# Kernel tuning notes

Hardware: AMD Instinct MI355X
Metric: run time of the kernel (lower is better)

The kernel has to match this reference:

```python
import jax, jax.numpy as jnp
import numpy as np

N = 131072   # number of points
C = 128      # channels
H = 8        # heads
D = C // H   # head dim = 16
K = 48       # patch (window) size
P = 3000     # number of path segments


def _build_indices():
    """Faithful numpy replica of PathAttention.get_padding_and_inverse (index-only, no_grad)."""
    rng = np.random.default_rng(0)
    lengths = rng.integers(K + 1, 3 * K, size=P)          # all > K -> padded to multiple of K
    M = int(lengths.sum())
    bpad = ((lengths + K - 1) // K) * K
    off = np.concatenate([[0], np.cumsum(lengths)])
    offp = np.concatenate([[0], np.cumsum(bpad)])
    Mpad = int(offp[-1])
    pad = np.arange(Mpad)
    unpad = np.arange(M)
    for i in range(P):
        o0, o1, p0, p1 = off[i], off[i + 1], offp[i], offp[i + 1]
        unpad[o0:o1] += p0 - o0
        b = int(lengths[i])
        if b != bpad[i]:
            r = b % K
            # replicate previous window's tail into the padded region
            pad[p1 - K + r:p1] = pad[p1 - 2 * K + r:p1 - K]
        pad[p0:p1] -= p0 - o0
    # every point appears at least once so the scatter-mean covers all N rows
    inv = np.concatenate([rng.permutation(N), rng.integers(0, N, M - N)])
    rng.shuffle(inv)
    return pad, unpad, inv


def setup_inputs() -> dict:
    pad, unpad, inv = _build_indices()
    M = unpad.shape[0]
    key = jax.random.key(0)
    ks = jax.random.split(key, 8)
    s = 0.02
    theta = jax.random.uniform(ks[1], (M, D), minval=0.0, maxval=2.0 * np.pi)
    return {
        "feat": jax.random.normal(ks[0], (N, C), jnp.float32),
        "cos": jnp.cos(theta).astype(jnp.float32),
        "sin": jnp.sin(theta).astype(jnp.float32),
        "g1": jnp.ones((C,), jnp.float32),
        "b1": jnp.zeros((C,), jnp.float32),
        "qkv_w": (jax.random.normal(ks[2], (3 * C, C)) * s).astype(jnp.float32),
        "qkv_b": jnp.zeros((3 * C,), jnp.float32),
        "proj_w": (jax.random.normal(ks[3], (C, C)) * s).astype(jnp.float32),
        "proj_b": jnp.zeros((C,), jnp.float32),
        "g2": jnp.ones((C,), jnp.float32),
        "b2": jnp.zeros((C,), jnp.float32),
        "fc1_w": (jax.random.normal(ks[4], (4 * C, C)) * s).astype(jnp.float32),
        "fc1_b": jnp.zeros((4 * C,), jnp.float32),
        "fc2_w": (jax.random.normal(ks[5], (C, 4 * C)) * s).astype(jnp.float32),
        "fc2_b": jnp.zeros((C,), jnp.float32),
        "path_inverse": jnp.asarray(inv, jnp.int32),
        "pad": jnp.asarray(pad, jnp.int32),
        "unpad": jnp.asarray(unpad, jnp.int32),
        "num_heads": H,
        "patch_size": K,
    }


def _ln(x, g, b):
    m = x.mean(-1, keepdims=True)
    v = x.var(-1, keepdims=True)
    return (x - m) / jnp.sqrt(v + 1e-5) * g + b


def reference(feat, cos, sin, g1, b1, qkv_w, qkv_b, proj_w, proj_b, g2, b2,
              fc1_w, fc1_b, fc2_w, fc2_b, path_inverse, pad, unpad,
              num_heads, patch_size):
    Np, Cc = feat.shape
    Hh = num_heads
    Dd = Cc // Hh
    Kk = patch_size
    # pre-norm + qkv projection, then path gather and pad gather
    h = _ln(feat, g1, b1)
    qkv = (h @ qkv_w.T + qkv_b)[path_inverse][pad]          # [Mpad, 3C]
    Mpad = qkv.shape[0]
    qkv = qkv.reshape(Mpad, 3, Hh, Dd)
    q, k, v = qkv[:, 0], qkv[:, 1], qkv[:, 2]               # [Mpad, H, D]
    # non-interleaved rope (flash-attn apply_rotary_emb with cos of dim D//2)
    cp = cos[pad][:, :Dd // 2][:, None, :]                  # [Mpad, 1, D/2]
    sp = sin[pad][:, :Dd // 2][:, None, :]
    def rope(x):
        x1, x2 = x[..., :Dd // 2], x[..., Dd // 2:]
        return jnp.concatenate([x1 * cp - x2 * sp, x2 * cp + x1 * sp], axis=-1)
    q = rope(q)
    k = rope(k)
    # windowed attention: all windows are exactly K after padding
    Wn = Mpad // Kk
    qw = q.reshape(Wn, Kk, Hh, Dd)
    kw = k.reshape(Wn, Kk, Hh, Dd)
    vw = v.reshape(Wn, Kk, Hh, Dd)
    scores = jnp.einsum('wqhd,wkhd->whqk', qw, kw) * (Dd ** -0.5)
    p = jax.nn.softmax(scores, axis=-1)
    o = jnp.einsum('whqk,wkhd->wqhd', p, vw).reshape(Mpad, Cc)
    # unpad gather, output projection, scatter-mean combine over overlapping paths
    o = o[unpad] @ proj_w.T + proj_b                        # [M, C]
    sums = jax.ops.segment_sum(o, path_inverse, num_segments=Np)
    cnt = jax.ops.segment_sum(jnp.ones((o.shape[0],), o.dtype), path_inverse, num_segments=Np)
    a = sums / jnp.maximum(cnt, 1.0)[:, None]
    x = feat + a
    # MLP branch
    h2 = _ln(x, g2, b2)
    m = jax.nn.gelu(h2 @ fc1_w.T + fc1_b, approximate=False) @ fc2_w.T + fc2_b
    return x + m
```

## Files before the change

### kernel.cpp

```cpp
#include <hip/hip_runtime.h>


typedef __attribute__((ext_vector_type(4))) float f32x4;
typedef __attribute__((ext_vector_type(8))) short bf16x8;
typedef __attribute__((ext_vector_type(4))) short bf16x4;
typedef __attribute__((ext_vector_type(2))) unsigned u32x2;

#define MFMA(a, b, c) __builtin_amdgcn_mfma_f32_16x16x32_bf16(a, b, c, 0, 0, 0)

static __device__ __forceinline__ short f2bf(float x) {
  union { float f; unsigned u; } v; v.f = x;
  unsigned r = v.u + 0x7FFFu + ((v.u >> 16) & 1u);
  return (short)(r >> 16);
}
static __device__ __forceinline__ float bf2f(short b) {
  union { unsigned u; float f; } v;
  v.u = ((unsigned)(unsigned short)b) << 16;
  return v.f;
}
static __device__ __forceinline__ unsigned cvt_pk_bf16(float lo, float hi) {
  unsigned r;
  asm("v_cvt_pk_bf16_f32 %0, %1, %2" : "=v"(r) : "v"(lo), "v"(hi));
  return r;
}
static __device__ __forceinline__ float exp2_f(float x) {
  float r; asm("v_exp_f32 %0, %1" : "=v"(r) : "v"(x)); return r;
}
static __device__ __forceinline__ float max3_f(float a, float b, float c) {
  float r; asm("v_max3_f32 %0, %1, %2, %3" : "=v"(r) : "v"(a), "v"(b), "v"(c));
  return r;
}

static __device__ __forceinline__ float gelu_f(float v) {
  float e = exp2_f(v * -2.4554669f);
  return v * __builtin_amdgcn_rcpf(1.0f + e);
}

__global__ void k_cvt(const float* __restrict__ s, short* __restrict__ d, int n) {
  int i = blockIdx.x * 256 + threadIdx.x;
  if (i < n) d[i] = f2bf(s[i]);
}

__global__ void k_pack_w1(const float* __restrict__ w, short* __restrict__ d) {
  int i = blockIdx.x * 256 + threadIdx.x;
  int j = i & 7;  int r = i >> 3;
  int g = r & 3;  r >>= 2;
  int u = r & 15; r >>= 4;
  int kk = r & 3; int t = r >> 2;
  d[i] = f2bf(w[(t * 16 + u) * 128 + kk * 32 + g * 8 + j]);
}

__global__ void k_pack_b1(const float* __restrict__ b, float* __restrict__ d) {
  int i = blockIdx.x * 256 + threadIdx.x;
  if (i < 512) {
    int reg = i & 3; int r = i >> 2;
    int g = r & 3;   int t = r >> 2;
    d[i] = b[16 * t + 4 * g + reg];
  }
}

__global__ void k_cnt(const int* __restrict__ pinv, int* __restrict__ cnt, int M) {
  int i = blockIdx.x * 256 + threadIdx.x;
  if (i < M) atomicAdd(&cnt[pinv[i]], 1);
}

__global__ __launch_bounds__(256) void k_scan1(const int* __restrict__ cnt,
                                               int* __restrict__ lpre,
                                               int* __restrict__ bsum) {
  const int i = blockIdx.x * 256 + threadIdx.x;
  const int t = threadIdx.x, lane = t & 63, wid = t >> 6;
  int v = cnt[i];
  int x = v;
#pragma unroll
  for (int d = 1; d < 64; d <<= 1) {
    int y = __shfl_up(x, d);
    if (lane >= d) x += y;
  }
  __shared__ int wsum[4];
  if (lane == 63) wsum[wid] = x;
  __syncthreads();
  int add = 0;
#pragma unroll
  for (int wv = 0; wv < 4; wv++) add += (wv < wid) ? wsum[wv] : 0;
  lpre[i] = x + add - v;
  if (t == 255) bsum[blockIdx.x] = x + add;
}

__global__ __launch_bounds__(512) void k_scan2(int* __restrict__ bsum, int nb) {
  const int t = threadIdx.x, lane = t & 63, wid = t >> 6;
  int v = (t < nb) ? bsum[t] : 0;
  int x = v;
#pragma unroll
  for (int d = 1; d < 64; d <<= 1) {
    int y = __shfl_up(x, d);
    if (lane >= d) x += y;
  }
  __shared__ int wsum[8];
  if (lane == 63) wsum[wid] = x;
  __syncthreads();
  int add = 0;
#pragma unroll
  for (int wv = 0; wv < 8; wv++) add += (wv < wid) ? wsum[wv] : 0;
  if (t < nb) bsum[t] = x + add - v;
}

__global__ void k_place(const int* __restrict__ pinv, const int* __restrict__ lpre,
                        const int* __restrict__ bsum, int* __restrict__ cursor,
                        int* __restrict__ idxl, int M) {
  int m = blockIdx.x * 256 + threadIdx.x;
  if (m < M) {
    int n = pinv[m];
    int slot = atomicAdd(&cursor[n], 1);
    idxl[lpre[n] + bsum[n >> 8] + slot] = m;
  }
}

__global__ __launch_bounds__(256) void k1_ln_qkv(
    const float* __restrict__ feat, const float* __restrict__ g1,
    const float* __restrict__ b1, const short* __restrict__ wq,
    const float* __restrict__ bq, short* __restrict__ qkvb) {
  __shared__ short h_lds[32 * 128];
  __shared__ short o_st[32 * 384];
  const int blk = blockIdx.x, t = threadIdx.x;
  {
    const int r = t >> 3, oct = t & 7;
    const float* fp = feat + (size_t)(blk * 32 + r) * 128 + oct * 16;
    float vals[16];
    float s = 0.f, s2 = 0.f;
#pragma unroll
    for (int i = 0; i < 4; i++) {
      f32x4 v = *(const f32x4*)(fp + i * 4);
#pragma unroll
      for (int j = 0; j < 4; j++) { float x = v[j]; vals[i * 4 + j] = x; s += x; s2 += x * x; }
    }
    s += __shfl_xor(s, 1);  s += __shfl_xor(s, 2);  s += __shfl_xor(s, 4);
    s2 += __shfl_xor(s2, 1); s2 += __shfl_xor(s2, 2); s2 += __shfl_xor(s2, 4);
    float mean = s * (1.f / 128.f);
    float rstd = rsqrtf(s2 * (1.f / 128.f) - mean * mean + 1e-5f);
    const int sw = (r & 7) << 4;
#pragma unroll
    for (int gi = 0; gi < 2; gi++) {
      bf16x8 wv;
#pragma unroll
      for (int j = 0; j < 8; j++) {
        int c = oct * 16 + gi * 8 + j;
        wv[j] = f2bf((vals[gi * 8 + j] - mean) * rstd * g1[c] + b1[c]);
      }
      *(bf16x8*)((char*)h_lds + r * 256 + ((oct * 32 + gi * 16) ^ sw)) = wv;
    }
  }
  __syncthreads();
  const int wave = t >> 6, lane = t & 63, u = lane & 15, g = lane >> 4;
  f32x4 acc[2][6];
  f32x4 zz = {0.f, 0.f, 0.f, 0.f};
#pragma unroll
  for (int a = 0; a < 2; a++)
#pragma unroll
    for (int b = 0; b < 6; b++) acc[a][b] = zz;
#pragma unroll
  for (int kk = 0; kk < 4; kk++) {
    bf16x8 af[2];
#pragma unroll
    for (int rt = 0; rt < 2; rt++)
      af[rt] = *(const bf16x8*)((char*)h_lds + (rt * 16 + u) * 256 +
                                ((kk * 64 + g * 16) ^ ((u & 7) << 4)));
    bf16x8 bfr[6];
#pragma unroll
    for (int ct = 0; ct < 6; ct++) {
      int col = wave * 96 + ct * 16 + u;
      bfr[ct] = *(const bf16x8*)(wq + (size_t)col * 128 + kk * 32 + g * 8);
    }
#pragma unroll
    for (int rt = 0; rt < 2; rt++)
#pragma unroll
      for (int ct = 0; ct < 6; ct++) acc[rt][ct] = MFMA(af[rt], bfr[ct], acc[rt][ct]);
  }
#pragma unroll
  for (int rt = 0; rt < 2; rt++)
#pragma unroll
    for (int ct = 0; ct < 6; ct++) {
      int col = wave * 96 + ct * 16 + u;
      float bias = bq[col];
#pragma unroll
      for (int reg = 0; reg < 4; reg++) {
        int rowl = rt * 16 + 4 * g + reg;
        *(short*)((char*)o_st + rowl * 768 + ((col * 2) ^ (g << 5))) =
            f2bf(acc[rt][ct][reg] + bias);
      }
    }
  __syncthreads();
  for (int idx = t; idx < 1536; idx += 256) {
    int r = idx / 48, c8 = idx % 48;
    bf16x8 v = *(const bf16x8*)((char*)o_st + r * 768 +
                                ((c8 * 16) ^ ((((r >> 2) & 3)) << 5)));
    *(bf16x8*)(qkvb + ((size_t)blk * 32 + r) * 384 + c8 * 8) = v;
  }
}

__global__ __launch_bounds__(512) void k2_attn(
    const short* __restrict__ qkv, const float* __restrict__ cosb,
    const float* __restrict__ sinb, const int* __restrict__ pinv,
    const int* __restrict__ padv, const int* __restrict__ unpadv,
    short* __restrict__ ocmp) {
  __shared__ short qo_lds[48 * 136];
  __shared__ short k_lds[48 * 128];
  __shared__ short vT[8 * 16 * 64];
  __shared__ int midx_s[48];
  __shared__ int gidx_s[48];
  __shared__ int canon_s[48];
  __shared__ float cs_s[48 * 8];
  __shared__ float sn_s[48 * 8];

  const int w = blockIdx.x;
  const int t = threadIdx.x;

  if (t < 48) {
    int pp = w * 48 + t;
    int m = padv[pp];
    midx_s[t] = m;
    gidx_s[t] = pinv[m];
    canon_s[t] = (unpadv[m] == pp) ? 1 : 0;
    const float* cp = cosb + (size_t)m * 16;
    const float* sp = sinb + (size_t)m * 16;
#pragma unroll
    for (int i = 0; i < 2; i++) {
      *(f32x4*)(cs_s + t * 8 + i * 4) = *(const f32x4*)(cp + i * 4);
      *(f32x4*)(sn_s + t * 8 + i * 4) = *(const f32x4*)(sp + i * 4);
    }
  }
  __syncthreads();

  {
    const int r = t >> 3, seg = t & 7;
    if (r < 48) {
      const short* rowp = qkv + (size_t)gidx_s[r] * 384;
      const float* cpr = cs_s + r * 8;
      const float* spr = sn_s + r * 8;
#pragma unroll
      for (int ci = 0; ci < 3; ci++) {
        const int c0 = seg * 48 + ci * 16;
        const int sec = c0 >> 7;
        const int hh = (c0 & 127) >> 4;
        bf16x8 lo = *(const bf16x8*)(rowp + c0);
        bf16x8 hi = *(const bf16x8*)(rowp + c0 + 8);
        if (sec < 2) {
          union { unsigned d[4]; bf16x8 v; } w0, w1;
#pragma unroll
          for (int j2 = 0; j2 < 4; j2++) {
            float x1a = bf2f(lo[2 * j2]),     x1b = bf2f(lo[2 * j2 + 1]);
            float x2a = bf2f(hi[2 * j2]),     x2b = bf2f(hi[2 * j2 + 1]);
            float ca = cpr[2 * j2], cb = cpr[2 * j2 + 1];
            float sa = spr[2 * j2], sb = spr[2 * j2 + 1];
            w0.d[j2] = cvt_pk_bf16(x1a * ca - x2a * sa, x1b * cb - x2b * sb);
            w1.d[j2] = cvt_pk_bf16(fmaf(x2a, ca, x1a * sa), fmaf(x2b, cb, x1b * sb));
          }
          char* dst = (char*)(sec == 0 ? qo_lds : k_lds);
          int sw = (r & 7) << 4;
          *(bf16x8*)(dst + r * 256 + ((hh * 32) ^ sw)) = w0.v;
          *(bf16x8*)(dst + r * 256 + ((hh * 32 + 16) ^ sw)) = w1.v;
        } else {
#pragma unroll
          for (int d = 0; d < 16; d++) {
            short val = (d < 8) ? lo[d] : hi[d - 8];
            *(short*)((char*)vT + hh * 2048 + d * 128 + ((r * 2) ^ ((d & 7) << 3))) = val;
          }
        }
      }
    } else {
#pragma unroll
      for (int ci = 0; ci < 3; ci++) {
        const int c0 = seg * 48 + ci * 16;
        if (c0 >= 256) {
          const int hh = (c0 & 127) >> 4;
#pragma unroll
          for (int d = 0; d < 16; d++)
            *(short*)((char*)vT + hh * 2048 + d * 128 + ((r * 2) ^ ((d & 7) << 3))) = 0;
        }
      }
    }
  }
  __syncthreads();

  const int h = t >> 6, lane = t & 63, u = lane & 15, g = lane >> 4;
  const int sbase = h * 32 + g * 16;
  bf16x8 zf = {0, 0, 0, 0, 0, 0, 0, 0};
  bf16x8 kf[3], qf[3];
#pragma unroll
  for (int i = 0; i < 3; i++) {
    int kj = i * 16 + u;
    if (g < 2) {
      kf[i] = *(const bf16x8*)((char*)k_lds + kj * 256 + (sbase ^ ((kj & 7) << 4)));
      qf[i] = *(const bf16x8*)((char*)qo_lds + kj * 256 + (sbase ^ ((kj & 7) << 4)));
    } else { kf[i] = zf; qf[i] = zf; }
  }
  union UU { bf16x8 v8; bf16x4 v4[2]; unsigned d[4]; };
  UU a1, a2;
  {
    const int dbase = h * 2048 + u * 128;
    const int sw = (u & 7) << 3;
    a1.v4[0] = *(const bf16x4*)((char*)vT + dbase + ((8 * g) ^ sw));
    a1.v4[1] = *(const bf16x4*)((char*)vT + dbase + ((32 + 8 * g) ^ sw));
    a2.v4[0] = *(const bf16x4*)((char*)vT + dbase + ((64 + 8 * g) ^ sw));
    a2.v4[1] = *(const bf16x4*)((char*)vT + dbase + ((96 + 8 * g) ^ sw));
  }
  __syncthreads();

  f32x4 d1[3][3];
#pragma unroll
  for (int a = 0; a < 3; a++)
#pragma unroll
    for (int b = 0; b < 3; b++) {
      f32x4 z = {0.f, 0.f, 0.f, 0.f};
      d1[a][b] = MFMA(kf[a], qf[b], z);
    }

  const float C = 0.36067376022224085f;
  float rl[3];
#pragma unroll
  for (int qt = 0; qt < 3; qt++) {
    float mx = max3_f(d1[0][qt][0], d1[0][qt][1], d1[0][qt][2]);
    mx = max3_f(mx, d1[0][qt][3], d1[1][qt][0]);
    mx = max3_f(mx, d1[1][qt][1], d1[1][qt][2]);
    mx = max3_f(mx, d1[1][qt][3], d1[2][qt][0]);
    mx = max3_f(mx, d1[2][qt][1], d1[2][qt][2]);
    mx = fmaxf(mx, d1[2][qt][3]);
    mx = fmaxf(mx, __shfl_xor(mx, 16));
    mx = fmaxf(mx, __shfl_xor(mx, 32));
    const float nb = -mx * C;
    float sm = 0.f;
#pragma unroll
    for (int kt = 0; kt < 3; kt++)
#pragma unroll
      for (int rr = 0; rr < 4; rr++) {
        float e = exp2_f(fmaf(d1[kt][qt][rr], C, nb));
        d1[kt][qt][rr] = e;
        sm += e;
      }
    sm += __shfl_xor(sm, 16);
    sm += __shfl_xor(sm, 32);
    rl[qt] = __builtin_amdgcn_rcpf(sm);
  }

#pragma unroll
  for (int qt = 0; qt < 3; qt++) {
    UU bu1, bu2;
    bu1.d[0] = cvt_pk_bf16(d1[0][qt][0], d1[0][qt][1]);
    bu1.d[1] = cvt_pk_bf16(d1[0][qt][2], d1[0][qt][3]);
    bu1.d[2] = cvt_pk_bf16(d1[1][qt][0], d1[1][qt][1]);
    bu1.d[3] = cvt_pk_bf16(d1[1][qt][2], d1[1][qt][3]);
    bu2.d[0] = cvt_pk_bf16(d1[2][qt][0], d1[2][qt][1]);
    bu2.d[1] = cvt_pk_bf16(d1[2][qt][2], d1[2][qt][3]);
    bu2.d[2] = 0; bu2.d[3] = 0;
    f32x4 z = {0.f, 0.f, 0.f, 0.f};
    f32x4 acc = MFMA(a1.v8, bu1.v8, z);
    acc = MFMA(a2.v8, bu2.v8, acc);
    const float rq = rl[qt];
    u32x2 ov;
    ov[0] = cvt_pk_bf16(acc[0] * rq, acc[1] * rq);
    ov[1] = cvt_pk_bf16(acc[2] * rq, acc[3] * rq);
    *(u32x2*)((char*)qo_lds + (qt * 16 + u) * 272 + h * 32 + g * 8) = ov;
  }
  __syncthreads();
  for (int idx = t; idx < 768; idx += 512) {
    int r = idx >> 4, c8 = idx & 15;
    if (canon_s[r]) {
      *(bf16x8*)(ocmp + (size_t)midx_s[r] * 128 + c8 * 8) =
          *(const bf16x8*)((char*)qo_lds + r * 272 + c8 * 16);
    }
  }
}

__global__ __launch_bounds__(256) void k3_proj(
    const short* __restrict__ ocmp, const short* __restrict__ wp,
    const float* __restrict__ pb, short* __restrict__ oproj, int M) {
  __shared__ short o_st[64 * 128];
  const int blk = blockIdx.x, t = threadIdx.x;
  const int m0 = blk * 64;
  const int wave = t >> 6, lane = t & 63, u = lane & 15, g = lane >> 4;
  f32x4 acc[4][2];
  f32x4 zz = {0.f, 0.f, 0.f, 0.f};
#pragma unroll
  for (int a = 0; a < 4; a++) { acc[a][0] = zz; acc[a][1] = zz; }
  bf16x8 zf = {0, 0, 0, 0, 0, 0, 0, 0};
#pragma unroll
  for (int kk = 0; kk < 4; kk++) {
    bf16x8 af[4];
#pragma unroll
    for (int rt = 0; rt < 4; rt++) {
      int m = m0 + rt * 16 + u;
      af[rt] = (m < M) ? *(const bf16x8*)(ocmp + (size_t)m * 128 + kk * 32 + g * 8) : zf;
    }
    bf16x8 bfr[2];
#pragma unroll
    for (int ct = 0; ct < 2; ct++) {
      int col = wave * 32 + ct * 16 + u;
      bfr[ct] = *(const bf16x8*)(wp + (size_t)col * 128 + kk * 32 + g * 8);
    }
#pragma unroll
    for (int rt = 0; rt < 4; rt++)
#pragma unroll
      for (int ct = 0; ct < 2; ct++) acc[rt][ct] = MFMA(af[rt], bfr[ct], acc[rt][ct]);
  }
#pragma unroll
  for (int rt = 0; rt < 4; rt++)
#pragma unroll
    for (int ct = 0; ct < 2; ct++) {
      int col = wave * 32 + ct * 16 + u;
      float bias = pb[col];
#pragma unroll
      for (int reg = 0; reg < 4; reg++) {
        int rowl = rt * 16 + 4 * g + reg;
        *(short*)((char*)o_st + rowl * 256 + ((col * 2) ^ (g << 5))) =
            f2bf(acc[rt][ct][reg] + bias);
      }
    }
  __syncthreads();
#pragma unroll
  for (int it = 0; it < 4; it++) {
    int idx = t + it * 256;
    int r = idx >> 4, c8 = idx & 15;
    if (m0 + r < M) {
      bf16x8 v = *(const bf16x8*)((char*)o_st + r * 256 +
                                  ((c8 * 16) ^ (((r >> 2) & 3) << 5)));
      *(bf16x8*)(oproj + (size_t)(m0 + r) * 128 + c8 * 8) = v;
    }
  }
}

__global__ __launch_bounds__(256) void k4a_gather_ln(
    const float* __restrict__ feat, float* __restrict__ dout,
    const int* __restrict__ cnt, const int* __restrict__ lpre,
    const int* __restrict__ bsum, const int* __restrict__ idxl,
    const short* __restrict__ oproj,
    const float* __restrict__ g2, const float* __restrict__ b2,
    short* __restrict__ hbuf) {
  const int t = threadIdx.x;
  const int r = t >> 3, oct = t & 7;
  const int n = blockIdx.x * 32 + r;
  const int c = cnt[n];
  const int start = lpre[n] + bsum[n >> 8];
  float sum[16];
#pragma unroll
  for (int i = 0; i < 16; i++) sum[i] = 0.f;
  for (int j = 0; j < c; j++) {
    int m = idxl[start + j];
    const short* op = oproj + (size_t)m * 128 + oct * 16;
    bf16x8 v0 = *(const bf16x8*)op;
    bf16x8 v1 = *(const bf16x8*)(op + 8);
#pragma unroll
    for (int q = 0; q < 8; q++) { sum[q] += bf2f(v0[q]); sum[8 + q] += bf2f(v1[q]); }
  }
  const float rc = 1.0f / fmaxf((float)c, 1.0f);
  const float* fp = feat + (size_t)n * 128 + oct * 16;
  float* xp = dout + (size_t)n * 128 + oct * 16;
  float vals[16];
  float s = 0.f, s2 = 0.f;
#pragma unroll
  for (int i = 0; i < 4; i++) {
    f32x4 fv = *(const f32x4*)(fp + i * 4);
    f32x4 xv;
#pragma unroll
    for (int j = 0; j < 4; j++) {
      float x = fv[j] + sum[i * 4 + j] * rc;
      xv[j] = x; vals[i * 4 + j] = x; s += x; s2 += x * x;
    }
    *(f32x4*)(xp + i * 4) = xv;
  }
  s += __shfl_xor(s, 1);  s += __shfl_xor(s, 2);  s += __shfl_xor(s, 4);
  s2 += __shfl_xor(s2, 1); s2 += __shfl_xor(s2, 2); s2 += __shfl_xor(s2, 4);
  float mean = s * (1.f / 128.f);
  float rstd = rsqrtf(s2 * (1.f / 128.f) - mean * mean + 1e-5f);
  bf16x8 h0, h1;
#pragma unroll
  for (int j = 0; j < 8; j++) {
    int c0 = oct * 16 + j, c1 = oct * 16 + 8 + j;
    h0[j] = f2bf((vals[j] - mean) * rstd * g2[c0] + b2[c0]);
    h1[j] = f2bf((vals[8 + j] - mean) * rstd * g2[c1] + b2[c1]);
  }
  short* hp = hbuf + (size_t)n * 128 + oct * 16;
  *(bf16x8*)hp = h0;
  *(bf16x8*)(hp + 8) = h1;
}

__global__ __launch_bounds__(256) void k4b1_fc1(
    const short* __restrict__ hbuf, const short* __restrict__ w1p,
    const float* __restrict__ b1p, short* __restrict__ p0,
    short* __restrict__ p1, int R0) {
  const int blk = blockIdx.x, t = threadIdx.x;
  const int wave = t >> 6, lane = t & 63, u = lane & 15, g = lane >> 4;
  const int row0 = blk * 64 + wave * 16;
  const int row = row0 + u;

  bf16x8 hf[4];
#pragma unroll
  for (int kk = 0; kk < 4; kk++)
    hf[kk] = *(const bf16x8*)(hbuf + (size_t)row * 128 + kk * 32 + g * 8);

  short* dstrow = (row0 < R0) ? (p0 + (size_t)row * 512)
                              : (p1 + ((size_t)(row - R0)) * 512);
#pragma unroll 4
  for (int tt = 0; tt < 32; tt++) {
    f32x4 acc = *(const f32x4*)(b1p + (tt * 4 + g) * 4);
#pragma unroll
    for (int kk = 0; kk < 4; kk++) {
      bf16x8 w1f = *(const bf16x8*)(w1p + (size_t)((tt * 4 + kk) * 64 +
                                                   u * 4 + g) * 8);
      acc = MFMA(w1f, hf[kk], acc);
    }
    u32x2 pv;
    pv[0] = cvt_pk_bf16(gelu_f(acc[0]), gelu_f(acc[1]));
    pv[1] = cvt_pk_bf16(gelu_f(acc[2]), gelu_f(acc[3]));
    *(u32x2*)(dstrow + tt * 16 + g * 4) = pv;
  }
}

__global__ __launch_bounds__(256, 4) void k4b2_fc2(
    const short* __restrict__ p0, const short* __restrict__ p1, int R0,
    const short* __restrict__ w2, const float* __restrict__ bb2,
    float* __restrict__ dout) {
  const int blk = blockIdx.x, t = threadIdx.x;
  const int row0 = blk * 64;
  const short* pb_ = (row0 < R0) ? (p0 + (size_t)row0 * 512)
                                 : (p1 + (size_t)(row0 - R0) * 512);
  const int wave = t >> 6, lane = t & 63, u = lane & 15, g = lane >> 4;
  f32x4 acc[4][2];
  f32x4 zz = {0.f, 0.f, 0.f, 0.f};
#pragma unroll
  for (int a = 0; a < 4; a++) { acc[a][0] = zz; acc[a][1] = zz; }

  auto ld_af = [&](bf16x8 (&af)[4], int kk) {
#pragma unroll
    for (int rt = 0; rt < 4; rt++)
      af[rt] = *(const bf16x8*)(pb_ + (size_t)(rt * 16 + u) * 512 +
                                kk * 32 + g * 8);
  };
  auto ld_bf = [&](bf16x8 (&bf)[2], int kk) {
#pragma unroll
    for (int ct = 0; ct < 2; ct++)
      bf[ct] = *(const bf16x8*)(w2 + (size_t)(wave * 32 + ct * 16 + u) * 512 +
                                kk * 32 + g * 8);
  };
  auto do_mfma = [&](bf16x8 (&af)[4], bf16x8 (&bf)[2]) {
#pragma unroll
    for (int rt = 0; rt < 4; rt++)
#pragma unroll
      for (int ct = 0; ct < 2; ct++) acc[rt][ct] = MFMA(af[rt], bf[ct], acc[rt][ct]);
  };

  bf16x8 afA[4], bfA[2], afB[4], bfB[2];
  ld_af(afA, 0); ld_bf(bfA, 0);
  ld_af(afB, 1); ld_bf(bfB, 1);
#pragma unroll
  for (int k2 = 0; k2 < 7; k2++) {
    do_mfma(afA, bfA);
    ld_af(afA, 2 * k2 + 2); ld_bf(bfA, 2 * k2 + 2);
    do_mfma(afB, bfB);
    ld_af(afB, 2 * k2 + 3); ld_bf(bfB, 2 * k2 + 3);
  }
  do_mfma(afA, bfA);
  do_mfma(afB, bfB);

#pragma unroll
  for (int rt = 0; rt < 4; rt++)
#pragma unroll
    for (int ct = 0; ct < 2; ct++) {
      int col = wave * 32 + ct * 16 + u;
      float bias = bb2[col];
#pragma unroll
      for (int reg = 0; reg < 4; reg++) {
        size_t rr = (size_t)row0 + rt * 16 + 4 * g + reg;
        float* p = dout + rr * 128 + col;
        *p = *p + acc[rt][ct][reg] + bias;
      }
    }
}

extern "C" void kernel_launch(void* const* d_in, const int* in_sizes, int n_in,
                              void* d_out, int out_size, void* d_ws, size_t ws_size,
                              hipStream_t stream) {
  (void)n_in; (void)out_size; (void)ws_size;
  const float* feat   = (const float*)d_in[0];
  const float* cosb   = (const float*)d_in[1];
  const float* sinb   = (const float*)d_in[2];
  const float* g1     = (const float*)d_in[3];
  const float* b1     = (const float*)d_in[4];
  const float* qkv_w  = (const float*)d_in[5];
  const float* qkv_b  = (const float*)d_in[6];
  const float* proj_w = (const float*)d_in[7];
  const float* proj_b = (const float*)d_in[8];
  const float* g2     = (const float*)d_in[9];
  const float* b2     = (const float*)d_in[10];
  const float* fc1_w  = (const float*)d_in[11];
  const float* fc1_b  = (const float*)d_in[12];
  const float* fc2_w  = (const float*)d_in[13];
  const float* fc2_b  = (const float*)d_in[14];
  const int* pinv     = (const int*)d_in[15];
  const int* padv     = (const int*)d_in[16];
  const int* unpadv   = (const int*)d_in[17];

  const int N    = in_sizes[0] / 128;
  const int M    = in_sizes[15];
  const int Mpad = in_sizes[16];
  const int Wn   = Mpad / 48;
  const int R0   = (N / 4) * 3;

  float* dout = (float*)d_out;
  char* ws = (char*)d_ws;

  size_t szQ = (size_t)N * 384 * 2;
  size_t szO = (size_t)M * 128 * 2;

  short* qkvb  = (short*)ws;
  short* oproj = (short*)ws;
  short* p0    = (short*)ws;
  short* ocmp  = (short*)(ws + szQ);
  short* hbuf  = (short*)(ws + szQ);
  short* p1    = (short*)(ws + szQ + (size_t)N * 256);

  size_t offI = ((size_t)M * 256 + 255) & ~(size_t)255;
  int* cnt    = (int*)(ws + offI);
  int* cursor = cnt + N;
  int* lpre   = cursor + N;
  int* bsum   = lpre + N;
  int* idxl   = bsum + 1024;

  size_t offW = szQ + szO;
  short* wq_b = (short*)(ws + offW);
  short* wp_b = wq_b + 49152;
  short* w1p  = wp_b + 16384;
  short* w2_b = w1p + 65536;
  float* b1p  = (float*)(w2_b + 65536);

  k_cvt<<<(49152 + 255) / 256, 256, 0, stream>>>(qkv_w, wq_b, 49152);
  k_cvt<<<(16384 + 255) / 256, 256, 0, stream>>>(proj_w, wp_b, 16384);
  k_pack_w1<<<256, 256, 0, stream>>>(fc1_w, w1p);
  k_cvt<<<(65536 + 255) / 256, 256, 0, stream>>>(fc2_w, w2_b, 65536);
  k_pack_b1<<<2, 256, 0, stream>>>(fc1_b, b1p);

  k1_ln_qkv<<<N / 32, 256, 0, stream>>>(feat, g1, b1, wq_b, qkv_b, qkvb);
  k2_attn<<<Wn, 512, 0, stream>>>(qkvb, cosb, sinb, pinv, padv, unpadv, ocmp);

  hipMemsetAsync(cnt, 0, (size_t)N * 4, stream);
  hipMemsetAsync(cursor, 0, (size_t)N * 4, stream);
  k_cnt<<<(M + 255) / 256, 256, 0, stream>>>(pinv, cnt, M);
  k_scan1<<<N / 256, 256, 0, stream>>>(cnt, lpre, bsum);
  k_scan2<<<1, 512, 0, stream>>>(bsum, N / 256);
  k_place<<<(M + 255) / 256, 256, 0, stream>>>(pinv, lpre, bsum, cursor, idxl, M);

  k3_proj<<<(M + 63) / 64, 256, 0, stream>>>(ocmp, wp_b, proj_b, oproj, M);
  k4a_gather_ln<<<N / 32, 256, 0, stream>>>(feat, dout, cnt, lpre, bsum, idxl,
                                            oproj, g2, b2, hbuf);
  k4b1_fc1<<<N / 64, 256, 0, stream>>>(hbuf, w1p, b1p, p0, p1, R0);
  k4b2_fc2<<<N / 64, 256, 0, stream>>>(p0, p1, R0, w2_b, fc2_b, dout);
}
```

Measured before the change: 506.8 us.

## Stage fc2 activation tiles into LDS with async global_load_lds double buffering

The fc2 kernel used to load its activation fragments straight from global memory into registers. It now copies 64x128 bf16 chunks into a double-buffered shared-memory tile with global_load_lds, using an XOR swizzle to avoid bank conflicts, and reads the MFMA A-operands from LDS. The four waves share the activation tile instead of each fetching it separately, which cuts redundant global traffic. In exchange it adds two block barriers per k-step and 32KB of LDS, which can reduce occupancy, and the launch-bounds occupancy hint is dropped.

```diff
diff --git a/kernel.cpp b/kernel.cpp
--- a/kernel.cpp
+++ b/kernel.cpp
@@ -29,6 +29,11 @@
 static __device__ __forceinline__ float max3_f(float a, float b, float c) {
   float r; asm("v_max3_f32 %0, %1, %2, %3" : "=v"(r) : "v"(a), "v"(b), "v"(c));
   return r;
+}
+static __device__ __forceinline__ void gload_lds16(const void* g, void* l) {
+  __builtin_amdgcn_global_load_lds(
+      (const __attribute__((address_space(1))) void*)g,
+      (__attribute__((address_space(3))) void*)l, 16, 0, 0);
 }
 
 static __device__ __forceinline__ float gelu_f(float v) {
@@ -514,51 +519,60 @@
   }
 }
 
-__global__ __launch_bounds__(256, 4) void k4b2_fc2(
+__global__ __launch_bounds__(256) void k4b2_fc2(
     const short* __restrict__ p0, const short* __restrict__ p1, int R0,
     const short* __restrict__ w2, const float* __restrict__ bb2,
     float* __restrict__ dout) {
+  __shared__ __align__(16) char tile[2][16384];
   const int blk = blockIdx.x, t = threadIdx.x;
   const int row0 = blk * 64;
   const short* pb_ = (row0 < R0) ? (p0 + (size_t)row0 * 512)
                                  : (p1 + (size_t)(row0 - R0) * 512);
   const int wave = t >> 6, lane = t & 63, u = lane & 15, g = lane >> 4;
+
+  auto stage = [&](int b, int ks) {
+#pragma unroll
+    for (int it = 0; it < 4; it++) {
+      int ci = (it * 4 + wave) * 64 + lane;
+      int r = ci >> 4, c = ci & 15;
+      const short* gp = pb_ + (size_t)r * 512 + ks * 128 + ((c ^ (r & 7)) * 8);
+      gload_lds16(gp, &tile[b][(it * 4 + wave) * 1024]);
+    }
+  };
+
   f32x4 acc[4][2];
   f32x4 zz = {0.f, 0.f, 0.f, 0.f};
 #pragma unroll
   for (int a = 0; a < 4; a++) { acc[a][0] = zz; acc[a][1] = zz; }
 
-  auto ld_af = [&](bf16x8 (&af)[4], int kk) {
-#pragma unroll
-    for (int rt = 0; rt < 4; rt++)
-      af[rt] = *(const bf16x8*)(pb_ + (size_t)(rt * 16 + u) * 512 +
-                                kk * 32 + g * 8);
-  };
-  auto ld_bf = [&](bf16x8 (&bf)[2], int kk) {
-#pragma unroll
-    for (int ct = 0; ct < 2; ct++)
-      bf[ct] = *(const bf16x8*)(w2 + (size_t)(wave * 32 + ct * 16 + u) * 512 +
-                                kk * 32 + g * 8);
-  };
-  auto do_mfma = [&](bf16x8 (&af)[4], bf16x8 (&bf)[2]) {
-#pragma unroll
-    for (int rt = 0; rt < 4; rt++)
-#pragma unroll
-      for (int ct = 0; ct < 2; ct++) acc[rt][ct] = MFMA(af[rt], bf[ct], acc[rt][ct]);
-  };
-
-  bf16x8 afA[4], bfA[2], afB[4], bfB[2];
-  ld_af(afA, 0); ld_bf(bfA, 0);
-  ld_af(afB, 1); ld_bf(bfB, 1);
-#pragma unroll
-  for (int k2 = 0; k2 < 7; k2++) {
-    do_mfma(afA, bfA);
-    ld_af(afA, 2 * k2 + 2); ld_bf(bfA, 2 * k2 + 2);
-    do_mfma(afB, bfB);
-    ld_af(afB, 2 * k2 + 3); ld_bf(bfB, 2 * k2 + 3);
-  }
-  do_mfma(afA, bfA);
-  do_mfma(afB, bfB);
+  stage(0, 0);
+#pragma unroll
+  for (int ks = 0; ks < 4; ks++) {
+    const int b = ks & 1;
+    bf16x8 bfr[4][2];
+#pragma unroll
+    for (int kk = 0; kk < 4; kk++)
+#pragma unroll
+      for (int ct = 0; ct < 2; ct++)
+        bfr[kk][ct] = *(const bf16x8*)(w2 + (size_t)(wave * 32 + ct * 16 + u) * 512 +
+                                       ks * 128 + kk * 32 + g * 8);
+    if (ks < 3) stage(b ^ 1, ks + 1);
+    __syncthreads();
+#pragma unroll
+    for (int kk = 0; kk < 4; kk++) {
+      bf16x8 af[4];
+#pragma unroll
+      for (int rt = 0; rt < 4; rt++)
+        af[rt] = *(const bf16x8*)(&tile[b][(rt * 16 + u) * 256 +
+                                           (((kk * 4 + g) ^ (u & 7)) * 16)]);
+#pragma unroll
+      for (int rt = 0; rt < 4; rt++)
+#pragma unroll
+        for (int ct = 0; ct < 2; ct++)
+          acc[rt][ct] = MFMA(af[rt], bfr[kk][ct], acc[rt][ct]);
+    }
+    __syncthreads();
+  }
 
 #pragma unroll
   for (int rt = 0; rt < 4; rt++)
```

Result: faster. 480.2 us (-5.2%).
